# Performance work log

Measured on AMD Instinct MI355X. Metric: run time of the kernel, lower is better.

Reference implementation:

```python
import jax, jax.numpy as jnp
import numpy as np


def setup_inputs() -> dict:
    key = jax.random.key(0)
    k1, k2 = jax.random.split(key)
    B, D, T_ENC, T_DEC = 16, 256, 512, 2048
    x = jax.random.normal(k1, (B, D, T_ENC), dtype=jnp.float32)
    path = jax.random.uniform(k2, (B, T_ENC, T_DEC), dtype=jnp.float32)
    return {"x": x, "path": path}


def reference(x, path):
    # Batched matmul: [B, D, T_enc] @ [B, T_enc, T_dec] -> [B, D, T_dec]
    return jnp.einsum('bde,bet->bdt', x, path)
```

## Files before the change

kernel.cpp:

```cpp
#include <hip/hip_runtime.h>
#include <hip/hip_bf16.h>

#define NB 16
#define ND 256
#define NK 512
#define NT 2048

#define BM 128
#define BN 128
#define BK 32
#define RSA 40
#define RSB 36

typedef __attribute__((ext_vector_type(8))) short short8;
typedef __attribute__((ext_vector_type(4))) float f32x4;

union S8U { short8 v; uint2 u[2]; };
union BF2U { __hip_bfloat162 h; unsigned int u; };

__device__ inline unsigned int pack2bf(float a, float b) {
    BF2U c; c.h = __float22bfloat162_rn(make_float2(a, b));
    return c.u;
}

__global__ __launch_bounds__(256, 2)
void bmm_bf16_mfma(const float* __restrict__ x, const float* __restrict__ path,
                   float* __restrict__ out) {
    const int id  = blockIdx.x;
    const int swz = (id & 7) * 64 + (id >> 3);
    const int b   = swz >> 5;
    const int rem = swz & 31;
    const int n0  = (rem >> 1) * BN;
    const int m0  = (rem & 1)  * BM;

    const int t    = threadIdx.x;
    const int lane = t & 63;
    const int wv   = t >> 6;
    const int wr   = (wv >> 1) * 64;
    const int wc   = (wv & 1) * 64;
    const int q    = lane >> 4;
    const int lm   = lane & 15;

    __shared__ unsigned short As[BM * RSA];
    __shared__ unsigned short Bs[BN * RSB];

    const float* xg = x    + ((size_t)b * ND + m0) * NK;
    const float* pg = path + (size_t)b * NK * NT + n0;

    f32x4 acc[4][4];
#pragma unroll
    for (int i = 0; i < 4; ++i)
#pragma unroll
        for (int j = 0; j < 4; ++j)
            acc[i][j] = (f32x4){0.f, 0.f, 0.f, 0.f};

    for (int k0 = 0; k0 < NK; k0 += BK) {
#pragma unroll
        for (int i = 0; i < 4; ++i) {
            int f   = t + i * 256;
            int row = f >> 3;
            int c4  = f & 7;
            float4 v = *reinterpret_cast<const float4*>(xg + (size_t)row * NK + k0 + c4 * 4);
            uint2 p;
            p.x = pack2bf(v.x, v.y);
            p.y = pack2bf(v.z, v.w);
            *reinterpret_cast<uint2*>(&As[row * RSA + c4 * 4]) = p;
        }
#pragma unroll
        for (int i = 0; i < 4; ++i) {
            int p   = wv * 4 + i;
            int kr4 = p >> 1;
            int ng  = p & 1;
            int n   = ng * 64 + lane;
            const float* src = pg + (size_t)(k0 + kr4 * 4) * NT + n;
            float f0 = src[0 * NT];
            float f1 = src[1 * NT];
            float f2 = src[2 * NT];
            float f3 = src[3 * NT];
            uint2 pk;
            pk.x = pack2bf(f0, f1);
            pk.y = pack2bf(f2, f3);
            *reinterpret_cast<uint2*>(&Bs[n * RSB + kr4 * 4]) = pk;
        }
        __syncthreads();

        short8 af[4];
        short8 bfr[4];
#pragma unroll
        for (int mt = 0; mt < 4; ++mt) {
            int row = wr + mt * 16 + lm;
            af[mt] = *reinterpret_cast<const short8*>(&As[row * RSA + q * 8]);
        }
#pragma unroll
        for (int nt = 0; nt < 4; ++nt) {
            int n = wc + nt * 16 + lm;
            S8U s;
            s.u[0] = *reinterpret_cast<const uint2*>(&Bs[n * RSB + q * 8]);
            s.u[1] = *reinterpret_cast<const uint2*>(&Bs[n * RSB + q * 8 + 4]);
            bfr[nt] = s.v;
        }
#pragma unroll
        for (int mt = 0; mt < 4; ++mt)
#pragma unroll
            for (int nt = 0; nt < 4; ++nt)
                acc[mt][nt] = __builtin_amdgcn_mfma_f32_16x16x32_bf16(
                    bfr[nt], af[mt], acc[mt][nt], 0, 0, 0);

        __syncthreads();
    }

    float* og = out + ((size_t)b * ND + m0 + wr) * NT + n0 + wc;
#pragma unroll
    for (int mt = 0; mt < 4; ++mt)
#pragma unroll
        for (int nt = 0; nt < 4; ++nt)
            *reinterpret_cast<f32x4*>(
                &og[(size_t)(mt * 16 + lm) * NT + nt * 16 + q * 4]) = acc[mt][nt];
}

extern "C" void kernel_launch(void* const* d_in, const int* in_sizes, int n_in,
                              void* d_out, int out_size, void* d_ws, size_t ws_size,
                              hipStream_t stream) {
    const float* x    = (const float*)d_in[0];
    const float* path = (const float*)d_in[1];
    float* out        = (float*)d_out;
    dim3 grid(512);
    dim3 block(256);
    bmm_bf16_mfma<<<grid, block, 0, stream>>>(x, path, out);
}
```

Measured before the change: 121.6 us.

## Double-buffer fp32 tiles via direct global-to-LDS loads with swizzle, convert at fragment read

Replaces register-staged loads with bf16 conversion before LDS by direct global_load_lds of raw fp32 tiles into a double-buffered, XOR-swizzled shared buffer. The conversion to bf16 now happens when MFMA fragments are read from LDS. The next tile's load is issued before the current tile's compute so the two overlap. It also drops the block-index swizzle in favor of a plain 3D grid. The cost is 64KB of LDS per block, which may limit occupancy to one block per CU with launch_bounds 2, plus more LDS traffic and conversion work in the inner loop.

```diff
diff --git a/kernel.cpp b/kernel.cpp
--- a/kernel.cpp
+++ b/kernel.cpp
@@ -9,30 +9,29 @@
 #define BM 128
 #define BN 128
 #define BK 32
-#define RSA 40
-#define RSB 36
+#define NSTEP (NK / BK)
 
 typedef __attribute__((ext_vector_type(8))) short short8;
 typedef __attribute__((ext_vector_type(4))) float f32x4;
 
-union S8U { short8 v; uint2 u[2]; };
 union BF2U { __hip_bfloat162 h; unsigned int u; };
+union S8U4 { short8 v; unsigned int u[4]; };
 
 __device__ inline unsigned int pack2bf(float a, float b) {
     BF2U c; c.h = __float22bfloat162_rn(make_float2(a, b));
     return c.u;
 }
 
+#define GLOAD_LDS(g, l) __builtin_amdgcn_global_load_lds(                     \
+    (const __attribute__((address_space(1))) void*)(g),                       \
+    (__attribute__((address_space(3))) void*)(l), 16, 0, 0)
+
 __global__ __launch_bounds__(256, 2)
 void bmm_bf16_mfma(const float* __restrict__ x, const float* __restrict__ path,
                    float* __restrict__ out) {
-    const int id  = blockIdx.x;
-    const int swz = (id & 7) * 64 + (id >> 3);
-    const int b   = swz >> 5;
-    const int rem = swz & 31;
-    const int n0  = (rem >> 1) * BN;
-    const int m0  = (rem & 1)  * BM;
-
+    const int n0 = blockIdx.x * BN;
+    const int m0 = blockIdx.y * BM;
+    const int b  = blockIdx.z;
     const int t    = threadIdx.x;
     const int lane = t & 63;
     const int wv   = t >> 6;
@@ -41,11 +40,39 @@
     const int q    = lane >> 4;
     const int lm   = lane & 15;
 
-    __shared__ unsigned short As[BM * RSA];
-    __shared__ unsigned short Bs[BN * RSB];
+    __shared__ float smem[2 * 8192];
 
     const float* xg = x    + ((size_t)b * ND + m0) * NK;
     const float* pg = path + (size_t)b * NK * NT + n0;
+
+    const float* gA[4]; const float* gB[4];
+    float* lA[4];       float* lB[4];
+#pragma unroll
+    for (int i = 0; i < 4; ++i) {
+        const int c  = wv * 4 + i;
+        const int ra = c * 8 + (lane >> 3);
+        const int sa = (lane & 7) ^ (ra & 7);
+        gA[i] = xg + (size_t)ra * NK + sa * 4;
+        lA[i] = &smem[c * 256];
+        const int kb = c * 2 + (lane >> 5);
+        const int sb = (lane & 31) ^ (((kb >> 3) & 1) << 2);
+        gB[i] = pg + (size_t)kb * NT + sb * 4;
+        lB[i] = &smem[4096 + c * 256];
+    }
+
+    auto stage = [&](int bo) {
+#pragma unroll
+        for (int i = 0; i < 4; ++i) { GLOAD_LDS(gA[i], lA[i] + bo); gA[i] += BK; }
+#pragma unroll
+        for (int i = 0; i < 4; ++i) { GLOAD_LDS(gB[i], lB[i] + bo); gB[i] += (size_t)BK * NT; }
+    };
+
+    const int vA0 = (wr + lm) * 32 + (((2 * q + 0) ^ (lm & 7)) * 4);
+    const int vA1 = (wr + lm) * 32 + (((2 * q + 1) ^ (lm & 7)) * 4);
+    int colB[4];
+#pragma unroll
+    for (int nt = 0; nt < 4; ++nt)
+        colB[nt] = wc + ((nt ^ (q & 1)) * 16) + lm;
 
     f32x4 acc[4][4];
 #pragma unroll
@@ -54,49 +81,29 @@
         for (int j = 0; j < 4; ++j)
             acc[i][j] = (f32x4){0.f, 0.f, 0.f, 0.f};
 
-    for (int k0 = 0; k0 < NK; k0 += BK) {
-#pragma unroll
-        for (int i = 0; i < 4; ++i) {
-            int f   = t + i * 256;
-            int row = f >> 3;
-            int c4  = f & 7;
-            float4 v = *reinterpret_cast<const float4*>(xg + (size_t)row * NK + k0 + c4 * 4);
-            uint2 p;
-            p.x = pack2bf(v.x, v.y);
-            p.y = pack2bf(v.z, v.w);
-            *reinterpret_cast<uint2*>(&As[row * RSA + c4 * 4]) = p;
-        }
-#pragma unroll
-        for (int i = 0; i < 4; ++i) {
-            int p   = wv * 4 + i;
-            int kr4 = p >> 1;
-            int ng  = p & 1;
-            int n   = ng * 64 + lane;
-            const float* src = pg + (size_t)(k0 + kr4 * 4) * NT + n;
-            float f0 = src[0 * NT];
-            float f1 = src[1 * NT];
-            float f2 = src[2 * NT];
-            float f3 = src[3 * NT];
-            uint2 pk;
-            pk.x = pack2bf(f0, f1);
-            pk.y = pack2bf(f2, f3);
-            *reinterpret_cast<uint2*>(&Bs[n * RSB + kr4 * 4]) = pk;
-        }
-        __syncthreads();
-
-        short8 af[4];
-        short8 bfr[4];
+    auto compute = [&](int bo) {
+        short8 afr[4], bfr[4];
 #pragma unroll
         for (int mt = 0; mt < 4; ++mt) {
-            int row = wr + mt * 16 + lm;
-            af[mt] = *reinterpret_cast<const short8*>(&As[row * RSA + q * 8]);
+            float4 x0 = *reinterpret_cast<const float4*>(&smem[bo + mt * 512 + vA0]);
+            float4 x1 = *reinterpret_cast<const float4*>(&smem[bo + mt * 512 + vA1]);
+            S8U4 s;
+            s.u[0] = pack2bf(x0.x, x0.y);
+            s.u[1] = pack2bf(x0.z, x0.w);
+            s.u[2] = pack2bf(x1.x, x1.y);
+            s.u[3] = pack2bf(x1.z, x1.w);
+            afr[mt] = s.v;
         }
 #pragma unroll
         for (int nt = 0; nt < 4; ++nt) {
-            int n = wc + nt * 16 + lm;
-            S8U s;
-            s.u[0] = *reinterpret_cast<const uint2*>(&Bs[n * RSB + q * 8]);
-            s.u[1] = *reinterpret_cast<const uint2*>(&Bs[n * RSB + q * 8 + 4]);
+            const float* bp = &smem[bo + 4096 + q * 1024 + colB[nt]];
+            float f0 = bp[0 * 128], f1 = bp[1 * 128], f2 = bp[2 * 128], f3 = bp[3 * 128];
+            float f4 = bp[4 * 128], f5 = bp[5 * 128], f6 = bp[6 * 128], f7 = bp[7 * 128];
+            S8U4 s;
+            s.u[0] = pack2bf(f0, f1);
+            s.u[1] = pack2bf(f2, f3);
+            s.u[2] = pack2bf(f4, f5);
+            s.u[3] = pack2bf(f6, f7);
             bfr[nt] = s.v;
         }
 #pragma unroll
@@ -104,8 +111,17 @@
 #pragma unroll
             for (int nt = 0; nt < 4; ++nt)
                 acc[mt][nt] = __builtin_amdgcn_mfma_f32_16x16x32_bf16(
-                    bfr[nt], af[mt], acc[mt][nt], 0, 0, 0);
+                    bfr[nt], afr[mt], acc[mt][nt], 0, 0, 0);
+    };
 
+    stage(0);
+    __syncthreads();
+    for (int p = 0; p < NSTEP / 2; ++p) {
+        stage(8192);
+        compute(0);
+        __syncthreads();
+        if (p < NSTEP / 2 - 1) stage(0);
+        compute(8192);
         __syncthreads();
     }
 
@@ -124,7 +140,7 @@
     const float* x    = (const float*)d_in[0];
     const float* path = (const float*)d_in[1];
     float* out        = (float*)d_out;
-    dim3 grid(512);
+    dim3 grid(NT / BN, ND / BM, NB);
     dim3 block(256);
     bmm_bf16_mfma<<<grid, block, 0, stream>>>(x, path, out);
 }
```

Result: slower. 125.2 us (+3.0%).

## Stream B tiles via async global-to-LDS loads with a 4-stage ring buffer

Applied to the files above, without the earlier changes.

Loads the fp32 path tile directly into shared memory with global_load_lds, using a four-buffer ring and three tiles in flight. The fp32-to-bf16 conversion of B moves from the producer into the fragment-building step, with an XOR swizzle on columns to avoid bank conflicts. The aim is to hide global memory latency for the larger B operand and stop spending registers and VALU work staging it. In exchange, shared memory use grows to about 64KB of fp32 B data per block, which may reduce occupancy. Each wave also does redundant conversions, and the hand-coded vmcnt waits and barriers must stay correct.

```diff
diff --git a/kernel.cpp b/kernel.cpp
--- a/kernel.cpp
+++ b/kernel.cpp
@@ -9,19 +9,30 @@
 #define BM 128
 #define BN 128
 #define BK 32
+#define NSTEP (NK / BK)
 #define RSA 40
-#define RSB 36
 
 typedef __attribute__((ext_vector_type(8))) short short8;
 typedef __attribute__((ext_vector_type(4))) float f32x4;
 
-union S8U { short8 v; uint2 u[2]; };
 union BF2U { __hip_bfloat162 h; unsigned int u; };
+union S8U4 { short8 v; unsigned int u[4]; };
 
 __device__ inline unsigned int pack2bf(float a, float b) {
     BF2U c; c.h = __float22bfloat162_rn(make_float2(a, b));
     return c.u;
 }
+
+#define GLOAD_LDS(g, l) __builtin_amdgcn_global_load_lds(                     \
+    (const __attribute__((address_space(1))) void*)(g),                       \
+    (__attribute__((address_space(3))) void*)(l), 16, 0, 0)
+
+#define VMCNT8() asm volatile("s_waitcnt vmcnt(8)" ::: "memory")
+#define VMCNT4() asm volatile("s_waitcnt vmcnt(4)" ::: "memory")
+#define VMCNT0() asm volatile("s_waitcnt vmcnt(0)" ::: "memory")
+#define LGKM0()  asm volatile("s_waitcnt lgkmcnt(0)" ::: "memory")
+#define BAR()    __builtin_amdgcn_s_barrier()
+#define SCHED0() __builtin_amdgcn_sched_barrier(0)
 
 __global__ __launch_bounds__(256, 2)
 void bmm_bf16_mfma(const float* __restrict__ x, const float* __restrict__ path,
@@ -42,19 +53,27 @@
     const int lm   = lane & 15;
 
     __shared__ unsigned short As[BM * RSA];
-    __shared__ unsigned short Bs[BN * RSB];
+    __shared__ float Bv[4 * 4096];
 
     const float* xg = x    + ((size_t)b * ND + m0) * NK;
     const float* pg = path + (size_t)b * NK * NT + n0;
 
-    f32x4 acc[4][4];
+    const float* gB[4];
+    float* lB[4];
 #pragma unroll
-    for (int i = 0; i < 4; ++i)
+    for (int i = 0; i < 4; ++i) {
+        const int c  = wv * 4 + i;
+        const int kb = c * 2 + (lane >> 5);
+        const int sb = (lane & 31) ^ (((kb >> 3) & 1) << 2);
+        gB[i] = pg + (size_t)kb * NT + sb * 4;
+        lB[i] = &Bv[c * 256];
+    }
+    auto stageB = [&](int bi) {
 #pragma unroll
-        for (int j = 0; j < 4; ++j)
-            acc[i][j] = (f32x4){0.f, 0.f, 0.f, 0.f};
+        for (int i = 0; i < 4; ++i) { GLOAD_LDS(gB[i], lB[i] + bi * 4096); gB[i] += (size_t)BK * NT; }
+    };
 
-    for (int k0 = 0; k0 < NK; k0 += BK) {
+    auto stageA = [&](int k0) {
 #pragma unroll
         for (int i = 0; i < 4; ++i) {
             int f   = t + i * 256;
@@ -66,37 +85,36 @@
             p.y = pack2bf(v.z, v.w);
             *reinterpret_cast<uint2*>(&As[row * RSA + c4 * 4]) = p;
         }
+    };
+
+    int colB[4];
 #pragma unroll
-        for (int i = 0; i < 4; ++i) {
-            int p   = wv * 4 + i;
-            int kr4 = p >> 1;
-            int ng  = p & 1;
-            int n   = ng * 64 + lane;
-            const float* src = pg + (size_t)(k0 + kr4 * 4) * NT + n;
-            float f0 = src[0 * NT];
-            float f1 = src[1 * NT];
-            float f2 = src[2 * NT];
-            float f3 = src[3 * NT];
-            uint2 pk;
-            pk.x = pack2bf(f0, f1);
-            pk.y = pack2bf(f2, f3);
-            *reinterpret_cast<uint2*>(&Bs[n * RSB + kr4 * 4]) = pk;
-        }
-        __syncthreads();
+    for (int nt = 0; nt < 4; ++nt)
+        colB[nt] = wc + ((nt ^ (q & 1)) * 16) + lm;
 
-        short8 af[4];
-        short8 bfr[4];
+    f32x4 acc[4][4];
 #pragma unroll
-        for (int mt = 0; mt < 4; ++mt) {
-            int row = wr + mt * 16 + lm;
-            af[mt] = *reinterpret_cast<const short8*>(&As[row * RSA + q * 8]);
-        }
+    for (int i = 0; i < 4; ++i)
+#pragma unroll
+        for (int j = 0; j < 4; ++j)
+            acc[i][j] = (f32x4){0.f, 0.f, 0.f, 0.f};
+
+    auto compute = [&](int bi) {
+        short8 af[4], bfr[4];
+#pragma unroll
+        for (int mt = 0; mt < 4; ++mt)
+            af[mt] = *reinterpret_cast<const short8*>(
+                &As[(wr + mt * 16 + lm) * RSA + q * 8]);
 #pragma unroll
         for (int nt = 0; nt < 4; ++nt) {
-            int n = wc + nt * 16 + lm;
-            S8U s;
-            s.u[0] = *reinterpret_cast<const uint2*>(&Bs[n * RSB + q * 8]);
-            s.u[1] = *reinterpret_cast<const uint2*>(&Bs[n * RSB + q * 8 + 4]);
+            const float* bp = &Bv[bi * 4096 + q * 1024 + colB[nt]];
+            float f0 = bp[0 * 128], f1 = bp[1 * 128], f2 = bp[2 * 128], f3 = bp[3 * 128];
+            float f4 = bp[4 * 128], f5 = bp[5 * 128], f6 = bp[6 * 128], f7 = bp[7 * 128];
+            S8U4 s;
+            s.u[0] = pack2bf(f0, f1);
+            s.u[1] = pack2bf(f2, f3);
+            s.u[2] = pack2bf(f4, f5);
+            s.u[3] = pack2bf(f6, f7);
             bfr[nt] = s.v;
         }
 #pragma unroll
@@ -105,9 +123,25 @@
             for (int nt = 0; nt < 4; ++nt)
                 acc[mt][nt] = __builtin_amdgcn_mfma_f32_16x16x32_bf16(
                     bfr[nt], af[mt], acc[mt][nt], 0, 0, 0);
+    };
 
-        __syncthreads();
+    stageB(0); stageB(1); stageB(2); SCHED0();
+
+    for (int s = 0; s < NSTEP - 3; ++s) {
+        VMCNT8(); SCHED0();
+        stageA(s * BK);
+        LGKM0();
+        BAR(); SCHED0();
+        stageB((s + 3) & 3);
+        compute(s & 3);
+        BAR(); SCHED0();
     }
+    VMCNT8(); SCHED0(); stageA(13 * BK); LGKM0(); BAR(); SCHED0();
+    compute(1); BAR(); SCHED0();
+    VMCNT4(); SCHED0(); stageA(14 * BK); LGKM0(); BAR(); SCHED0();
+    compute(2); BAR(); SCHED0();
+    VMCNT0(); SCHED0(); stageA(15 * BK); LGKM0(); BAR(); SCHED0();
+    compute(3);
 
     float* og = out + ((size_t)b * ND + m0 + wr) * NT + n0 + wc;
 #pragma unroll
```

Result: slower. 135.5 us (+11.5%).
